# Kernel tuning notes

Hardware: AMD Instinct MI355X
Metric: run time of the kernel (lower is better)

The kernel has to match this reference:

```python
import jax, jax.numpy as jnp
import numpy as np

EPS = 1e-5  # torch BatchNorm2d default eps


def setup_inputs() -> dict:
    key = jax.random.key(0)
    ks = jax.random.split(key, 11)
    n, c, h, w = 16, 512, 64, 64
    grp, cg, mip = 4, 128, 16
    return {
        "x": jax.random.normal(ks[0], (n, c, h, w), dtype=jnp.float32),
        "W1": jax.random.normal(ks[1], (mip, cg), dtype=jnp.float32) * 0.05,
        "b1": jax.random.normal(ks[2], (mip,), dtype=jnp.float32) * 0.05,
        "gamma": jax.random.uniform(ks[3], (mip,), dtype=jnp.float32, minval=0.5, maxval=1.5),
        "beta": jax.random.normal(ks[4], (mip,), dtype=jnp.float32) * 0.05,
        "mean": jax.random.normal(ks[5], (mip,), dtype=jnp.float32) * 0.05,
        "var": jax.random.uniform(ks[6], (mip,), dtype=jnp.float32, minval=0.5, maxval=1.5),
        "Wh": jax.random.normal(ks[7], (cg, mip), dtype=jnp.float32) * 0.1,
        "bh": jax.random.normal(ks[8], (cg,), dtype=jnp.float32) * 0.05,
        "Ww": jax.random.normal(ks[9], (cg, mip), dtype=jnp.float32) * 0.1,
        "bw": jax.random.normal(ks[10], (cg,), dtype=jnp.float32) * 0.05,
    }


def reference(x, W1, b1, gamma, beta, mean, var, Wh, bh, Ww, bw):
    n, c, h, w = x.shape
    grp = 4
    cg = c // grp
    # Since c % 4 == 0, torch.split gives 4 equal groups: fold group into a new axis.
    xg = x.reshape(n, grp, cg, h, w)                       # (n,g,cg,h,w)
    gh = xg.mean(axis=4)                                   # pool over w -> (n,g,cg,h)
    gw = xg.mean(axis=3)                                   # pool over h -> (n,g,cg,w)
    y = jnp.concatenate([gh, gw], axis=3)                  # (n,g,cg,h+w)
    # conv1 (1x1) shared across all 4 groups
    y = jnp.einsum('ngcl,mc->ngml', y, W1) + b1[None, None, :, None]
    # BatchNorm2d (eval mode, running stats)
    scale = gamma / jnp.sqrt(var + EPS)
    y = y * scale[None, None, :, None] + (beta - mean * scale)[None, None, :, None]
    # h_swish: x * relu6(x+3)/6
    y = y * (jnp.clip(y + 3.0, 0.0, 6.0) / 6.0)
    yh, yw = y[..., :h], y[..., h:]                        # (n,g,mip,h), (n,g,mip,w)
    a_h = jax.nn.sigmoid(jnp.einsum('ngml,cm->ngcl', yh, Wh) + bh[None, None, :, None])
    a_w = jax.nn.sigmoid(jnp.einsum('ngml,cm->ngcl', yw, Ww) + bw[None, None, :, None])
    out = xg * a_h[..., :, None] * a_w[..., None, :]       # (n,g,cg,h,w)
    out = out.reshape(n, c, h, w)
    # channel shuffle: (n, cg, grp, h, w) -> permute group axis forward
    out = out.reshape(n, cg, grp, h, w).transpose(0, 2, 1, 3, 4).reshape(n, c, h, w)
    return out
```

## Files before the change

### kernel.cpp

```cpp
#include <hip/hip_runtime.h>

#define N_   16
#define C_   512
#define GRP  4
#define CG   128
#define MIP  16

__device__ __forceinline__ float bf_lo(unsigned u) { return __uint_as_float(u << 16); }
__device__ __forceinline__ float bf_hi(unsigned u) { return __uint_as_float(u & 0xFFFF0000u); }
__device__ __forceinline__ float bf1(unsigned short s) { return __uint_as_float((unsigned)s << 16); }

__device__ __forceinline__ float ld_scalar(const void* p, int i, bool isbf) {
    return isbf ? bf1(((const unsigned short*)p)[i]) : ((const float*)p)[i];
}

__device__ __forceinline__ bool wave_sniff_isbf(const unsigned* __restrict__ x32,
                                                int lane) {
    int cnt = 0;
    #pragma unroll
    for (int k = 0; k < 4; ++k) {
        unsigned w = x32[lane + 64 * k];
        unsigned e = (w >> 7) & 0xFFu;
        cnt += (e >= 0x60u && e <= 0x9Fu) ? 1 : 0;
    }
    #pragma unroll
    for (int off = 32; off > 0; off >>= 1) cnt += __shfl_xor(cnt, off, 64);
    return cnt >= 192;
}

__device__ __forceinline__ bool sniff_isbf(const unsigned* __restrict__ x32,
                                           int t, unsigned* s_flag) {
    if (t < 64) {
        int cnt = 0;
        #pragma unroll
        for (int k = 0; k < 4; ++k) {
            unsigned w = x32[t + 64 * k];
            unsigned e = (w >> 7) & 0xFFu;
            cnt += (e >= 0x60u && e <= 0x9Fu) ? 1 : 0;
        }
        #pragma unroll
        for (int off = 32; off > 0; off >>= 1) cnt += __shfl_down(cnt, off, 64);
        if (t == 0) *s_flag = (cnt >= 192) ? 1u : 0u;
    }
    __syncthreads();
    return *s_flag != 0u;
}

__global__ __launch_bounds__(256) void kreduce(const void* __restrict__ xv,
                                               float* __restrict__ gh,
                                               float* __restrict__ gw) {
    const int lane = threadIdx.x & 63;
    const int gwid = blockIdx.x * 4 + (threadIdx.x >> 6);
    const bool isbf = wave_sniff_isbf((const unsigned*)xv, lane);

    #pragma unroll
    for (int j = 0; j < 2; ++j) {
        const int tile = gwid * 2 + j;
        if (isbf) {
            const uint4* src = (const uint4*)((const unsigned short*)xv + (size_t)tile * 4096);
            float cp[8] = {0,0,0,0,0,0,0,0};
            #pragma unroll
            for (int i = 0; i < 8; ++i) {
                uint4 v = src[i * 64 + lane];
                unsigned uu[4] = {v.x, v.y, v.z, v.w};
                float rp = 0.f;
                #pragma unroll
                for (int k = 0; k < 4; ++k) {
                    float f0 = bf_lo(uu[k]), f1 = bf_hi(uu[k]);
                    rp += f0 + f1;
                    cp[2*k] += f0; cp[2*k+1] += f1;
                }
                rp += __shfl_xor(rp, 1, 64);
                rp += __shfl_xor(rp, 2, 64);
                rp += __shfl_xor(rp, 4, 64);
                if ((lane & 7) == 0)
                    gh[(size_t)tile * 64 + i * 8 + (lane >> 3)] = rp * (1.f/64.f);
            }
            #pragma unroll
            for (int k = 0; k < 8; ++k) {
                cp[k] += __shfl_xor(cp[k], 8, 64);
                cp[k] += __shfl_xor(cp[k], 16, 64);
                cp[k] += __shfl_xor(cp[k], 32, 64);
            }
            if (lane < 8) {
                float4 a = make_float4(cp[0], cp[1], cp[2], cp[3]);
                float4 b = make_float4(cp[4], cp[5], cp[6], cp[7]);
                a.x *= (1.f/64.f); a.y *= (1.f/64.f); a.z *= (1.f/64.f); a.w *= (1.f/64.f);
                b.x *= (1.f/64.f); b.y *= (1.f/64.f); b.z *= (1.f/64.f); b.w *= (1.f/64.f);
                float4* dst = (float4*)(gw + (size_t)tile * 64 + lane * 8);
                dst[0] = a; dst[1] = b;
            }
        } else {
            const float4* src = (const float4*)((const float*)xv + (size_t)tile * 4096);
            float cp[4] = {0,0,0,0};
            #pragma unroll
            for (int i = 0; i < 16; ++i) {
                float4 v = src[i * 64 + lane];
                float rp = (v.x + v.y) + (v.z + v.w);
                cp[0] += v.x; cp[1] += v.y; cp[2] += v.z; cp[3] += v.w;
                rp += __shfl_xor(rp, 1, 64);
                rp += __shfl_xor(rp, 2, 64);
                rp += __shfl_xor(rp, 4, 64);
                rp += __shfl_xor(rp, 8, 64);
                if ((lane & 15) == 0)
                    gh[(size_t)tile * 64 + i * 4 + (lane >> 4)] = rp * (1.f/64.f);
            }
            #pragma unroll
            for (int k = 0; k < 4; ++k) {
                cp[k] += __shfl_xor(cp[k], 16, 64);
                cp[k] += __shfl_xor(cp[k], 32, 64);
            }
            if (lane < 16) {
                float4 a = make_float4(cp[0] * (1.f/64.f), cp[1] * (1.f/64.f),
                                       cp[2] * (1.f/64.f), cp[3] * (1.f/64.f));
                *(float4*)(gw + (size_t)tile * 64 + lane * 4) = a;
            }
        }
    }
}

__global__ __launch_bounds__(256) void kmid(
    const void* __restrict__ xv,
    const float* __restrict__ gh, const float* __restrict__ gw,
    const void* __restrict__ W1, const void* __restrict__ b1,
    const void* __restrict__ gamma, const void* __restrict__ beta,
    const void* __restrict__ mean, const void* __restrict__ var,
    const void* __restrict__ Wh, const void* __restrict__ bh,
    const void* __restrict__ Ww, const void* __restrict__ bw,
    float* __restrict__ aH, float* __restrict__ aW)
{
    __shared__ float W1_s[MIP * CG];
    __shared__ float Whw_s[2][CG * MIP];
    __shared__ float y_s[MIP * 128];
    __shared__ float bhw_s[2][CG];
    __shared__ float scale_s[MIP], shift_s[MIP], b1_s[MIP];
    __shared__ unsigned flag_s;

    const int t = threadIdx.x;
    const int ng = blockIdx.x;
    const bool isbf = sniff_isbf((const unsigned*)xv, t, &flag_s);

    if (isbf) {
        uint4 v = ((const uint4*)W1)[t];
        unsigned uu[4] = {v.x, v.y, v.z, v.w};
        #pragma unroll
        for (int k = 0; k < 4; ++k) {
            W1_s[t*8 + 2*k]   = bf_lo(uu[k]);
            W1_s[t*8 + 2*k+1] = bf_hi(uu[k]);
        }
        uint4 a = ((const uint4*)Wh)[t];
        unsigned ua[4] = {a.x, a.y, a.z, a.w};
        #pragma unroll
        for (int k = 0; k < 4; ++k) {
            Whw_s[0][t*8 + 2*k]   = bf_lo(ua[k]);
            Whw_s[0][t*8 + 2*k+1] = bf_hi(ua[k]);
        }
        uint4 c = ((const uint4*)Ww)[t];
        unsigned uc[4] = {c.x, c.y, c.z, c.w};
        #pragma unroll
        for (int k = 0; k < 4; ++k) {
            Whw_s[1][t*8 + 2*k]   = bf_lo(uc[k]);
            Whw_s[1][t*8 + 2*k+1] = bf_hi(uc[k]);
        }
    } else {
        #pragma unroll
        for (int it = 0; it < 2; ++it) {
            int idx = t + 256 * it;
            float4 v = ((const float4*)W1)[idx];
            W1_s[idx*4] = v.x; W1_s[idx*4+1] = v.y; W1_s[idx*4+2] = v.z; W1_s[idx*4+3] = v.w;
            float4 a = ((const float4*)Wh)[idx];
            Whw_s[0][idx*4] = a.x; Whw_s[0][idx*4+1] = a.y; Whw_s[0][idx*4+2] = a.z; Whw_s[0][idx*4+3] = a.w;
            float4 c = ((const float4*)Ww)[idx];
            Whw_s[1][idx*4] = c.x; Whw_s[1][idx*4+1] = c.y; Whw_s[1][idx*4+2] = c.z; Whw_s[1][idx*4+3] = c.w;
        }
    }
    if (t < CG) bhw_s[0][t] = ld_scalar(bh, t, isbf);
    else        bhw_s[1][t - CG] = ld_scalar(bw, t - CG, isbf);
    if (t < MIP) {
        float sc = ld_scalar(gamma, t, isbf) * rsqrtf(ld_scalar(var, t, isbf) + 1e-5f);
        scale_s[t] = sc;
        shift_s[t] = ld_scalar(beta, t, isbf) - ld_scalar(mean, t, isbf) * sc;
        b1_s[t] = ld_scalar(b1, t, isbf);
    }
    __syncthreads();

    {
        const int l = t & 127;
        const int half = t >> 7;
        const float* gbase = (l < 64) ? (gh + (size_t)ng * 8192 + l)
                                      : (gw + (size_t)ng * 8192 + (l - 64));
        float acc[8] = {0,0,0,0,0,0,0,0};
        for (int cc = 0; cc < CG; ++cc) {
            float v = gbase[(size_t)cc * 64];
            #pragma unroll
            for (int mm = 0; mm < 8; ++mm)
                acc[mm] += W1_s[(half*8 + mm) * CG + cc] * v;
        }
        #pragma unroll
        for (int mm = 0; mm < 8; ++mm) {
            int m = half*8 + mm;
            float yv = acc[mm] + b1_s[m];
            yv = yv * scale_s[m] + shift_s[m];
            float hc = fminf(fmaxf(yv + 3.f, 0.f), 6.f);
            y_s[m * 128 + l] = yv * hc * (1.f/6.f);
        }
    }
    __syncthreads();

    for (int k = 0; k < 64; ++k) {
        int out = t + 256 * k;
        int hf = out >> 13;
        int rem = out & 8191;
        int cc = rem >> 6;
        int i = rem & 63;
        float acc = bhw_s[hf][cc];
        #pragma unroll
        for (int m = 0; m < MIP; ++m)
            acc += Whw_s[hf][cc * MIP + m] * y_s[m * 128 + hf * 64 + i];
        float s = 1.f / (1.f + __expf(-acc));
        float* dst = hf ? aW : aH;
        dst[(size_t)ng * 8192 + cc * 64 + i] = s;
    }
}

__global__ __launch_bounds__(256) void kapply(const void* __restrict__ xv,
                                              const float* __restrict__ aH,
                                              const float* __restrict__ aW,
                                              void* __restrict__ outv) {
    const int lane = threadIdx.x & 63;
    const int gwid = blockIdx.x * 4 + (threadIdx.x >> 6);
    const bool isbf = wave_sniff_isbf((const unsigned*)xv, lane);

    #pragma unroll
    for (int j = 0; j < 2; ++j) {
        const int bid = gwid * 2 + j;
        const int n = bid >> 9;
        const int o = bid & 511;
        const int p = (o & 127) * 4 + (o >> 7);
        const int g = p >> 7, cc = p & 127;
        const size_t abase = (size_t)(n * 4 + g) * 8192 + (size_t)cc * 64;

        const float ah_r = aH[abase + lane];
        const float aw_r = aW[abase + lane];

        if (isbf) {
            float awv[8];
            #pragma unroll
            for (int k = 0; k < 8; ++k)
                awv[k] = __shfl(aw_r, (lane & 7) * 8 + k, 64);
            const uint4* src = (const uint4*)((const unsigned short*)xv + ((size_t)n * 512 + p) * 4096);
            uint4* dst = (uint4*)((unsigned short*)outv + (size_t)bid * 4096);
            #pragma unroll
            for (int i = 0; i < 8; ++i) {
                float sah = __shfl(ah_r, i * 8 + (lane >> 3), 64);
                uint4 v = src[i * 64 + lane];
                unsigned uu[4] = {v.x, v.y, v.z, v.w};
                unsigned res[4];
                #pragma unroll
                for (int k = 0; k < 4; ++k) {
                    float f0 = bf_lo(uu[k]) * sah * awv[2*k];
                    float f1 = bf_hi(uu[k]) * sah * awv[2*k+1];
                    unsigned u0 = __float_as_uint(f0); u0 += 0x7FFFu + ((u0 >> 16) & 1u);
                    unsigned u1 = __float_as_uint(f1); u1 += 0x7FFFu + ((u1 >> 16) & 1u);
                    res[k] = (u0 >> 16) | (u1 & 0xFFFF0000u);
                }
                uint4 w2; w2.x = res[0]; w2.y = res[1]; w2.z = res[2]; w2.w = res[3];
                dst[i * 64 + lane] = w2;
            }
        } else {
            float awv[4];
            #pragma unroll
            for (int k = 0; k < 4; ++k)
                awv[k] = __shfl(aw_r, (lane & 15) * 4 + k, 64);
            const float4* src = (const float4*)((const float*)xv + ((size_t)n * 512 + p) * 4096);
            float4* dst = (float4*)((float*)outv + (size_t)bid * 4096);
            #pragma unroll
            for (int i = 0; i < 16; ++i) {
                float sah = __shfl(ah_r, i * 4 + (lane >> 4), 64);
                float4 v = src[i * 64 + lane];
                v.x *= sah * awv[0];
                v.y *= sah * awv[1];
                v.z *= sah * awv[2];
                v.w *= sah * awv[3];
                dst[i * 64 + lane] = v;
            }
        }
    }
}

extern "C" void kernel_launch(void* const* d_in, const int* in_sizes, int n_in,
                              void* d_out, int out_size, void* d_ws, size_t ws_size,
                              hipStream_t stream) {
    const void* x     = d_in[0];
    const void* W1    = d_in[1];
    const void* b1    = d_in[2];
    const void* gamma = d_in[3];
    const void* beta  = d_in[4];
    const void* mean  = d_in[5];
    const void* var   = d_in[6];
    const void* Wh    = d_in[7];
    const void* bh    = d_in[8];
    const void* Ww    = d_in[9];
    const void* bw    = d_in[10];

    float* ws = (float*)d_ws;
    float* gh = ws;
    float* gw = gh + 524288;
    float* aH = gw + 524288;
    float* aW = aH + 524288;

    kreduce<<<1024, 256, 0, stream>>>(x, gh, gw);
    kmid<<<N_ * GRP, 256, 0, stream>>>(x, gh, gw, W1, b1, gamma, beta, mean, var,
                                       Wh, bh, Ww, bw, aH, aW);
    kapply<<<1024, 256, 0, stream>>>(x, aH, aW, d_out);
}
```

Baseline: 295.3 us.

## Fuse attention-weight conv and sigmoid into apply kernel, one tile per wave

The second 1x1 conv plus sigmoid for the h and w attention vectors moves out of the 64-block middle kernel and into the apply kernel, where each wave computes its own channel's 64+64 attention values from the small y buffer. This removes the serial 16K-output loop in a low-parallelism kernel and the aH/aW round trip through global memory. The reduce and apply kernels now process one tile per wave with twice as many blocks. In exchange, the Wh/Ww weights are re-read per wave with scalar loads, which adds a small amount of compute to the bandwidth-bound apply pass.

Result: faster. 286.4 us (-3.0%).

```diff
diff --git a/kernel.cpp b/kernel.cpp
--- a/kernel.cpp
+++ b/kernel.cpp
@@ -50,94 +50,84 @@
                                                float* __restrict__ gh,
                                                float* __restrict__ gw) {
     const int lane = threadIdx.x & 63;
-    const int gwid = blockIdx.x * 4 + (threadIdx.x >> 6);
+    const int tile = blockIdx.x * 4 + (threadIdx.x >> 6);
     const bool isbf = wave_sniff_isbf((const unsigned*)xv, lane);
 
-    #pragma unroll
-    for (int j = 0; j < 2; ++j) {
-        const int tile = gwid * 2 + j;
-        if (isbf) {
-            const uint4* src = (const uint4*)((const unsigned short*)xv + (size_t)tile * 4096);
-            float cp[8] = {0,0,0,0,0,0,0,0};
-            #pragma unroll
-            for (int i = 0; i < 8; ++i) {
-                uint4 v = src[i * 64 + lane];
-                unsigned uu[4] = {v.x, v.y, v.z, v.w};
-                float rp = 0.f;
-                #pragma unroll
-                for (int k = 0; k < 4; ++k) {
-                    float f0 = bf_lo(uu[k]), f1 = bf_hi(uu[k]);
-                    rp += f0 + f1;
-                    cp[2*k] += f0; cp[2*k+1] += f1;
-                }
-                rp += __shfl_xor(rp, 1, 64);
-                rp += __shfl_xor(rp, 2, 64);
-                rp += __shfl_xor(rp, 4, 64);
-                if ((lane & 7) == 0)
-                    gh[(size_t)tile * 64 + i * 8 + (lane >> 3)] = rp * (1.f/64.f);
-            }
-            #pragma unroll
-            for (int k = 0; k < 8; ++k) {
-                cp[k] += __shfl_xor(cp[k], 8, 64);
-                cp[k] += __shfl_xor(cp[k], 16, 64);
-                cp[k] += __shfl_xor(cp[k], 32, 64);
-            }
-            if (lane < 8) {
-                float4 a = make_float4(cp[0], cp[1], cp[2], cp[3]);
-                float4 b = make_float4(cp[4], cp[5], cp[6], cp[7]);
-                a.x *= (1.f/64.f); a.y *= (1.f/64.f); a.z *= (1.f/64.f); a.w *= (1.f/64.f);
-                b.x *= (1.f/64.f); b.y *= (1.f/64.f); b.z *= (1.f/64.f); b.w *= (1.f/64.f);
-                float4* dst = (float4*)(gw + (size_t)tile * 64 + lane * 8);
-                dst[0] = a; dst[1] = b;
-            }
-        } else {
-            const float4* src = (const float4*)((const float*)xv + (size_t)tile * 4096);
-            float cp[4] = {0,0,0,0};
-            #pragma unroll
-            for (int i = 0; i < 16; ++i) {
-                float4 v = src[i * 64 + lane];
-                float rp = (v.x + v.y) + (v.z + v.w);
-                cp[0] += v.x; cp[1] += v.y; cp[2] += v.z; cp[3] += v.w;
-                rp += __shfl_xor(rp, 1, 64);
-                rp += __shfl_xor(rp, 2, 64);
-                rp += __shfl_xor(rp, 4, 64);
-                rp += __shfl_xor(rp, 8, 64);
-                if ((lane & 15) == 0)
-                    gh[(size_t)tile * 64 + i * 4 + (lane >> 4)] = rp * (1.f/64.f);
-            }
+    if (isbf) {
+        const uint4* src = (const uint4*)((const unsigned short*)xv + (size_t)tile * 4096);
+        float cp[8] = {0,0,0,0,0,0,0,0};
+        #pragma unroll
+        for (int i = 0; i < 8; ++i) {
+            uint4 v = src[i * 64 + lane];
+            unsigned uu[4] = {v.x, v.y, v.z, v.w};
+            float rp = 0.f;
             #pragma unroll
             for (int k = 0; k < 4; ++k) {
-                cp[k] += __shfl_xor(cp[k], 16, 64);
-                cp[k] += __shfl_xor(cp[k], 32, 64);
+                float f0 = bf_lo(uu[k]), f1 = bf_hi(uu[k]);
+                rp += f0 + f1;
+                cp[2*k] += f0; cp[2*k+1] += f1;
             }
-            if (lane < 16) {
-                float4 a = make_float4(cp[0] * (1.f/64.f), cp[1] * (1.f/64.f),
-                                       cp[2] * (1.f/64.f), cp[3] * (1.f/64.f));
-                *(float4*)(gw + (size_t)tile * 64 + lane * 4) = a;
-            }
-        }
-    }
-}
-
-__global__ __launch_bounds__(256) void kmid(
+            rp += __shfl_xor(rp, 1, 64);
+            rp += __shfl_xor(rp, 2, 64);
+            rp += __shfl_xor(rp, 4, 64);
+            if ((lane & 7) == 0)
+                gh[(size_t)tile * 64 + i * 8 + (lane >> 3)] = rp * (1.f/64.f);
+        }
+        #pragma unroll
+        for (int k = 0; k < 8; ++k) {
+            cp[k] += __shfl_xor(cp[k], 8, 64);
+            cp[k] += __shfl_xor(cp[k], 16, 64);
+            cp[k] += __shfl_xor(cp[k], 32, 64);
+        }
+        if (lane < 8) {
+            float4 a = make_float4(cp[0]*(1.f/64.f), cp[1]*(1.f/64.f),
+                                   cp[2]*(1.f/64.f), cp[3]*(1.f/64.f));
+            float4 b = make_float4(cp[4]*(1.f/64.f), cp[5]*(1.f/64.f),
+                                   cp[6]*(1.f/64.f), cp[7]*(1.f/64.f));
+            float4* dst = (float4*)(gw + (size_t)tile * 64 + lane * 8);
+            dst[0] = a; dst[1] = b;
+        }
+    } else {
+        const float4* src = (const float4*)((const float*)xv + (size_t)tile * 4096);
+        float cp[4] = {0,0,0,0};
+        #pragma unroll
+        for (int i = 0; i < 16; ++i) {
+            float4 v = src[i * 64 + lane];
+            float rp = (v.x + v.y) + (v.z + v.w);
+            cp[0] += v.x; cp[1] += v.y; cp[2] += v.z; cp[3] += v.w;
+            rp += __shfl_xor(rp, 1, 64);
+            rp += __shfl_xor(rp, 2, 64);
+            rp += __shfl_xor(rp, 4, 64);
+            rp += __shfl_xor(rp, 8, 64);
+            if ((lane & 15) == 0)
+                gh[(size_t)tile * 64 + i * 4 + (lane >> 4)] = rp * (1.f/64.f);
+        }
+        #pragma unroll
+        for (int k = 0; k < 4; ++k) {
+            cp[k] += __shfl_xor(cp[k], 16, 64);
+            cp[k] += __shfl_xor(cp[k], 32, 64);
+        }
+        if (lane < 16) {
+            float4 a = make_float4(cp[0]*(1.f/64.f), cp[1]*(1.f/64.f),
+                                   cp[2]*(1.f/64.f), cp[3]*(1.f/64.f));
+            *(float4*)(gw + (size_t)tile * 64 + lane * 4) = a;
+        }
+    }
+}
+
+__global__ __launch_bounds__(256) void ky(
     const void* __restrict__ xv,
     const float* __restrict__ gh, const float* __restrict__ gw,
     const void* __restrict__ W1, const void* __restrict__ b1,
     const void* __restrict__ gamma, const void* __restrict__ beta,
     const void* __restrict__ mean, const void* __restrict__ var,
-    const void* __restrict__ Wh, const void* __restrict__ bh,
-    const void* __restrict__ Ww, const void* __restrict__ bw,
-    float* __restrict__ aH, float* __restrict__ aW)
+    float* __restrict__ y)
 {
     __shared__ float W1_s[MIP * CG];
-    __shared__ float Whw_s[2][CG * MIP];
-    __shared__ float y_s[MIP * 128];
-    __shared__ float bhw_s[2][CG];
     __shared__ float scale_s[MIP], shift_s[MIP], b1_s[MIP];
     __shared__ unsigned flag_s;
 
     const int t = threadIdx.x;
-    const int ng = blockIdx.x;
     const bool isbf = sniff_isbf((const unsigned*)xv, t, &flag_s);
 
     if (isbf) {
@@ -145,37 +135,20 @@
         unsigned uu[4] = {v.x, v.y, v.z, v.w};
         #pragma unroll
         for (int k = 0; k < 4; ++k) {
-            W1_s[t*8 + 2*k]   = bf_lo(uu[k]);
-            W1_s[t*8 + 2*k+1] = bf_hi(uu[k]);
-        }
-        uint4 a = ((const uint4*)Wh)[t];
-        unsigned ua[4] = {a.x, a.y, a.z, a.w};
-        #pragma unroll
-        for (int k = 0; k < 4; ++k) {
-            Whw_s[0][t*8 + 2*k]   = bf_lo(ua[k]);
-            Whw_s[0][t*8 + 2*k+1] = bf_hi(ua[k]);
-        }
-        uint4 c = ((const uint4*)Ww)[t];
-        unsigned uc[4] = {c.x, c.y, c.z, c.w};
-        #pragma unroll
-        for (int k = 0; k < 4; ++k) {
-            Whw_s[1][t*8 + 2*k]   = bf_lo(uc[k]);
-            Whw_s[1][t*8 + 2*k+1] = bf_hi(uc[k]);
+            W1_s[t * 8 + 2 * k]     = bf_lo(uu[k]);
+            W1_s[t * 8 + 2 * k + 1] = bf_hi(uu[k]);
         }
     } else {
         #pragma unroll
         for (int it = 0; it < 2; ++it) {
             int idx = t + 256 * it;
             float4 v = ((const float4*)W1)[idx];
-            W1_s[idx*4] = v.x; W1_s[idx*4+1] = v.y; W1_s[idx*4+2] = v.z; W1_s[idx*4+3] = v.w;
-            float4 a = ((const float4*)Wh)[idx];
-            Whw_s[0][idx*4] = a.x; Whw_s[0][idx*4+1] = a.y; Whw_s[0][idx*4+2] = a.z; Whw_s[0][idx*4+3] = a.w;
-            float4 c = ((const float4*)Ww)[idx];
-            Whw_s[1][idx*4] = c.x; Whw_s[1][idx*4+1] = c.y; Whw_s[1][idx*4+2] = c.z; Whw_s[1][idx*4+3] = c.w;
-        }
-    }
-    if (t < CG) bhw_s[0][t] = ld_scalar(bh, t, isbf);
-    else        bhw_s[1][t - CG] = ld_scalar(bw, t - CG, isbf);
+            W1_s[idx * 4]     = v.x;
+            W1_s[idx * 4 + 1] = v.y;
+            W1_s[idx * 4 + 2] = v.z;
+            W1_s[idx * 4 + 3] = v.w;
+        }
+    }
     if (t < MIP) {
         float sc = ld_scalar(gamma, t, isbf) * rsqrtf(ld_scalar(var, t, isbf) + 1e-5f);
         scale_s[t] = sc;
@@ -184,106 +157,97 @@
     }
     __syncthreads();
 
-    {
-        const int l = t & 127;
-        const int half = t >> 7;
-        const float* gbase = (l < 64) ? (gh + (size_t)ng * 8192 + l)
-                                      : (gw + (size_t)ng * 8192 + (l - 64));
-        float acc[8] = {0,0,0,0,0,0,0,0};
-        for (int cc = 0; cc < CG; ++cc) {
-            float v = gbase[(size_t)cc * 64];
-            #pragma unroll
-            for (int mm = 0; mm < 8; ++mm)
-                acc[mm] += W1_s[(half*8 + mm) * CG + cc] * v;
-        }
-        #pragma unroll
-        for (int mm = 0; mm < 8; ++mm) {
-            int m = half*8 + mm;
-            float yv = acc[mm] + b1_s[m];
-            yv = yv * scale_s[m] + shift_s[m];
-            float hc = fminf(fmaxf(yv + 3.f, 0.f), 6.f);
-            y_s[m * 128 + l] = yv * hc * (1.f/6.f);
-        }
-    }
-    __syncthreads();
-
-    for (int k = 0; k < 64; ++k) {
-        int out = t + 256 * k;
-        int hf = out >> 13;
-        int rem = out & 8191;
-        int cc = rem >> 6;
-        int i = rem & 63;
-        float acc = bhw_s[hf][cc];
-        #pragma unroll
-        for (int m = 0; m < MIP; ++m)
-            acc += Whw_s[hf][cc * MIP + m] * y_s[m * 128 + hf * 64 + i];
-        float s = 1.f / (1.f + __expf(-acc));
-        float* dst = hf ? aW : aH;
-        dst[(size_t)ng * 8192 + cc * 64 + i] = s;
+    const int l = t & 127;
+    const int half = t >> 7;
+    const size_t base = (size_t)blockIdx.x * (CG * 64);
+    const float* src = (l < 64) ? (gh + base + l) : (gw + base + (l - 64));
+    float acc[8] = {0.f, 0.f, 0.f, 0.f, 0.f, 0.f, 0.f, 0.f};
+    for (int cc = 0; cc < CG; ++cc) {
+        float v = src[(size_t)cc * 64];
+        #pragma unroll
+        for (int mm = 0; mm < 8; ++mm)
+            acc[mm] += W1_s[(half * 8 + mm) * CG + cc] * v;
+    }
+    float* yb = y + (size_t)blockIdx.x * (MIP * 128);
+    #pragma unroll
+    for (int mm = 0; mm < 8; ++mm) {
+        int m = half * 8 + mm;
+        float yv = acc[mm] + b1_s[m];
+        yv = yv * scale_s[m] + shift_s[m];
+        float hc = fminf(fmaxf(yv + 3.0f, 0.0f), 6.0f);
+        yb[m * 128 + l] = yv * hc * (1.0f / 6.0f);
     }
 }
 
 __global__ __launch_bounds__(256) void kapply(const void* __restrict__ xv,
-                                              const float* __restrict__ aH,
-                                              const float* __restrict__ aW,
+                                              const float* __restrict__ y,
+                                              const void* __restrict__ Wh,
+                                              const void* __restrict__ bh,
+                                              const void* __restrict__ Ww,
+                                              const void* __restrict__ bw,
                                               void* __restrict__ outv) {
     const int lane = threadIdx.x & 63;
-    const int gwid = blockIdx.x * 4 + (threadIdx.x >> 6);
+    const int bid = blockIdx.x * 4 + (threadIdx.x >> 6);
     const bool isbf = wave_sniff_isbf((const unsigned*)xv, lane);
 
-    #pragma unroll
-    for (int j = 0; j < 2; ++j) {
-        const int bid = gwid * 2 + j;
-        const int n = bid >> 9;
-        const int o = bid & 511;
-        const int p = (o & 127) * 4 + (o >> 7);
-        const int g = p >> 7, cc = p & 127;
-        const size_t abase = (size_t)(n * 4 + g) * 8192 + (size_t)cc * 64;
-
-        const float ah_r = aH[abase + lane];
-        const float aw_r = aW[abase + lane];
-
-        if (isbf) {
-            float awv[8];
+    const int n = bid >> 9;
+    const int o = bid & 511;
+    const int p = (o & 127) * 4 + (o >> 7);
+    const int g = p >> 7, cc = p & 127;
+
+    const float* ysrc = y + (size_t)(n * 4 + g) * (MIP * 128);
+    float acch = ld_scalar(bh, cc, isbf);
+    float accw = ld_scalar(bw, cc, isbf);
+    #pragma unroll
+    for (int m = 0; m < MIP; ++m) {
+        float wh = ld_scalar(Wh, cc * MIP + m, isbf);
+        float ww = ld_scalar(Ww, cc * MIP + m, isbf);
+        acch += wh * ysrc[m * 128 + lane];
+        accw += ww * ysrc[m * 128 + 64 + lane];
+    }
+    const float ah_r = 1.0f / (1.0f + __expf(-acch));
+    const float aw_r = 1.0f / (1.0f + __expf(-accw));
+
+    if (isbf) {
+        float awv[8];
+        #pragma unroll
+        for (int k = 0; k < 8; ++k)
+            awv[k] = __shfl(aw_r, (lane & 7) * 8 + k, 64);
+        const uint4* src = (const uint4*)((const unsigned short*)xv + ((size_t)n * 512 + p) * 4096);
+        uint4* dst = (uint4*)((unsigned short*)outv + (size_t)bid * 4096);
+        #pragma unroll
+        for (int i = 0; i < 8; ++i) {
+            float sah = __shfl(ah_r, i * 8 + (lane >> 3), 64);
+            uint4 v = src[i * 64 + lane];
+            unsigned uu[4] = {v.x, v.y, v.z, v.w};
+            unsigned res[4];
             #pragma unroll
-            for (int k = 0; k < 8; ++k)
-                awv[k] = __shfl(aw_r, (lane & 7) * 8 + k, 64);
-            const uint4* src = (const uint4*)((const unsigned short*)xv + ((size_t)n * 512 + p) * 4096);
-            uint4* dst = (uint4*)((unsigned short*)outv + (size_t)bid * 4096);
-            #pragma unroll
-            for (int i = 0; i < 8; ++i) {
-                float sah = __shfl(ah_r, i * 8 + (lane >> 3), 64);
-                uint4 v = src[i * 64 + lane];
-                unsigned uu[4] = {v.x, v.y, v.z, v.w};
-                unsigned res[4];
-                #pragma unroll
-                for (int k = 0; k < 4; ++k) {
-                    float f0 = bf_lo(uu[k]) * sah * awv[2*k];
-                    float f1 = bf_hi(uu[k]) * sah * awv[2*k+1];
-                    unsigned u0 = __float_as_uint(f0); u0 += 0x7FFFu + ((u0 >> 16) & 1u);
-                    unsigned u1 = __float_as_uint(f1); u1 += 0x7FFFu + ((u1 >> 16) & 1u);
-                    res[k] = (u0 >> 16) | (u1 & 0xFFFF0000u);
-                }
-                uint4 w2; w2.x = res[0]; w2.y = res[1]; w2.z = res[2]; w2.w = res[3];
-                dst[i * 64 + lane] = w2;
+            for (int k = 0; k < 4; ++k) {
+                float f0 = bf_lo(uu[k]) * sah * awv[2*k];
+                float f1 = bf_hi(uu[k]) * sah * awv[2*k+1];
+                unsigned u0 = __float_as_uint(f0); u0 += 0x7FFFu + ((u0 >> 16) & 1u);
+                unsigned u1 = __float_as_uint(f1); u1 += 0x7FFFu + ((u1 >> 16) & 1u);
+                res[k] = (u0 >> 16) | (u1 & 0xFFFF0000u);
             }
-        } else {
-            float awv[4];
-            #pragma unroll
-            for (int k = 0; k < 4; ++k)
-                awv[k] = __shfl(aw_r, (lane & 15) * 4 + k, 64);
-            const float4* src = (const float4*)((const float*)xv + ((size_t)n * 512 + p) * 4096);
-            float4* dst = (float4*)((float*)outv + (size_t)bid * 4096);
-            #pragma unroll
-            for (int i = 0; i < 16; ++i) {
-                float sah = __shfl(ah_r, i * 4 + (lane >> 4), 64);
-                float4 v = src[i * 64 + lane];
-                v.x *= sah * awv[0];
-                v.y *= sah * awv[1];
-                v.z *= sah * awv[2];
-                v.w *= sah * awv[3];
-                dst[i * 64 + lane] = v;
-            }
+            uint4 w2; w2.x = res[0]; w2.y = res[1]; w2.z = res[2]; w2.w = res[3];
+            dst[i * 64 + lane] = w2;
+        }
+    } else {
+        float awv[4];
+        #pragma unroll
+        for (int k = 0; k < 4; ++k)
+            awv[k] = __shfl(aw_r, (lane & 15) * 4 + k, 64);
+        const float4* src = (const float4*)((const float*)xv + ((size_t)n * 512 + p) * 4096);
+        float4* dst = (float4*)((float*)outv + (size_t)bid * 4096);
+        #pragma unroll
+        for (int i = 0; i < 16; ++i) {
+            float sah = __shfl(ah_r, i * 4 + (lane >> 4), 64);
+            float4 v = src[i * 64 + lane];
+            v.x *= sah * awv[0];
+            v.y *= sah * awv[1];
+            v.z *= sah * awv[2];
+            v.w *= sah * awv[3];
+            dst[i * 64 + lane] = v;
         }
     }
 }
@@ -306,11 +270,9 @@
     float* ws = (float*)d_ws;
     float* gh = ws;
     float* gw = gh + 524288;
-    float* aH = gw + 524288;
-    float* aW = aH + 524288;
-
-    kreduce<<<1024, 256, 0, stream>>>(x, gh, gw);
-    kmid<<<N_ * GRP, 256, 0, stream>>>(x, gh, gw, W1, b1, gamma, beta, mean, var,
-                                       Wh, bh, Ww, bw, aH, aW);
-    kapply<<<1024, 256, 0, stream>>>(x, aH, aW, d_out);
-}
+    float* yv = gw + 524288;
+
+    kreduce<<<2048, 256, 0, stream>>>(x, gh, gw);
+    ky<<<N_ * GRP, 256, 0, stream>>>(x, gh, gw, W1, b1, gamma, beta, mean, var, yv);
+    kapply<<<2048, 256, 0, stream>>>(x, yv, Wh, bh, Ww, bw, d_out);
+}
```
